# Kernel tuning notes

Measured on AMD Instinct MI355X. Metric: run time of the kernel, lower is better.

Reference implementation:

```python
import jax, jax.numpy as jnp
from jax import lax
import numpy as np

NEG = -1e9  # finite stand-in for -inf: keeps logaddexp grads NaN-free, exp underflows to 0
BLANK = 0
T_MAX, B, C = 256, 64, 8000
L_MAX = 32


def setup_inputs() -> dict:
    key = jax.random.key(0)
    k1, k2, k3, k4 = jax.random.split(key, 4)
    logits = jax.random.normal(k1, (T_MAX, B, C), dtype=jnp.float32)
    log_probs = jax.nn.log_softmax(logits, axis=-1)  # [T,B,C]
    targets = jax.random.randint(k2, (B, L_MAX), 1, C, dtype=jnp.int32)  # labels in [1,C), blank excluded
    input_lengths = jax.random.randint(k3, (B,), T_MAX // 2 + 1, T_MAX + 1, dtype=jnp.int32)
    target_lengths = jax.random.randint(k4, (B,), L_MAX // 2 + 1, L_MAX + 1, dtype=jnp.int32)
    return {"log_probs": log_probs, "targets": targets,
            "input_lengths": input_lengths, "target_lengths": target_lengths}


def _ctc_losses(log_probs, targets, input_lengths, target_lengths):
    T, Bb, Cc = log_probs.shape
    Lm = targets.shape[1]
    S = 2 * Lm + 1

    # extended targets: blank-interleaved labels, blank beyond 2L (matches torch buffer)
    lmask = jnp.arange(Lm)[None, :] < target_lengths[:, None]
    tgt = jnp.where(lmask, targets, BLANK)
    ext = jnp.full((Bb, S), BLANK, dtype=targets.dtype).at[:, 1::2].set(tgt)  # [B,S]

    ext_shift2 = jnp.concatenate(
        [jnp.full((Bb, 2), -1, dtype=ext.dtype), ext[:, :-2]], axis=1)
    skip = (ext != BLANK) & (ext != ext_shift2)  # [B,S]

    # emissions[t,b,s] = log_probs[t, b, ext[b,s]]
    emissions = jnp.take_along_axis(
        log_probs, jnp.broadcast_to(ext[None], (T, Bb, S)), axis=2)  # [T,B,S]

    # alpha init at t=0
    lp0 = log_probs[0]
    a0 = jnp.full((Bb, S), NEG, dtype=log_probs.dtype)
    a0 = a0.at[:, 0].set(lp0[:, BLANK])
    first_char = jnp.take_along_axis(lp0, ext[:, 1:2], axis=1)[:, 0]
    a0 = a0.at[:, 1].set(jnp.where(target_lengths > 0, first_char,
                                   jnp.full((Bb,), NEG, dtype=log_probs.dtype)))

    neg1 = jnp.full((Bb, 1), NEG, dtype=log_probs.dtype)
    neg2 = jnp.full((Bb, 2), NEG, dtype=log_probs.dtype)

    def step(alpha, em_t):
        p = jnp.logaddexp(alpha, jnp.concatenate([neg1, alpha[:, :-1]], axis=1))
        p = jnp.where(skip, jnp.logaddexp(p, jnp.concatenate([neg2, alpha[:, :-2]], axis=1)), p)
        new = p + em_t
        return new, new

    _, hist = lax.scan(step, a0, emissions[1:])
    alpha_hist = jnp.concatenate([a0[None], hist], axis=0)  # [T,B,S]

    final_alpha = alpha_hist[input_lengths - 1, jnp.arange(Bb)]  # [B,S]
    i_blank = 2 * target_lengths
    i_char = jnp.maximum(2 * target_lengths - 1, 0)
    v_blank = jnp.take_along_axis(final_alpha, i_blank[:, None], axis=1)[:, 0]
    v_char = jnp.take_along_axis(final_alpha, i_char[:, None], axis=1)[:, 0]
    total_log_prob = jnp.where(target_lengths > 0,
                               jnp.logaddexp(v_blank, v_char), v_blank)
    return -total_log_prob  # [B]


def reference(log_probs, targets, input_lengths, target_lengths):
    losses = _ctc_losses(log_probs, targets, input_lengths, target_lengths)
    safe_len = jnp.maximum(target_lengths, 1).astype(losses.dtype)
    return jnp.mean(losses / safe_len)  # reduction='mean'
```

## Files before the change

kernel.cpp:

```cpp
#include <hip/hip_runtime.h>
#include <cstdint>
#include <cstddef>


#define TMAX  256
#define BATCH 64
#define CNUM  8000
#define LMAX  32
#define SDIM  65
#define LOG2E 1.44269504088896340736f
#define LN2   0.69314718055994530942f
#define NEG2  (-1.0e9f * LOG2E)

__device__ __forceinline__ float hexp2(float x) { return __builtin_amdgcn_exp2f(x); }
__device__ __forceinline__ float hlog2(float x) { return __builtin_amdgcn_logf(x); }

__device__ __forceinline__ float lae3_log2(float a, float b, float c) {
    float m = fmaxf(fmaxf(a, b), c);
    float r = hexp2(a - m) + hexp2(b - m) + hexp2(c - m);
    return m + hlog2(r);
}

__global__ __launch_bounds__(256) void ctc_dp(
    const float* __restrict__ lp, const int* __restrict__ targets,
    const int* __restrict__ in_len, const int* __restrict__ tg_len,
    float* __restrict__ partial)
{
    const int b   = blockIdx.x;
    const int tid = threadIdx.x;
    const int Lb  = tg_len[b];
    const int Tb  = in_len[b];

    __shared__ float s_em[TMAX][LMAX + 1];

    {
        const int t = tid;
        const float* rowbase = lp + (size_t)t * (size_t)(BATCH * CNUM)
                                  + (size_t)b * CNUM;
        s_em[t][LMAX] = rowbase[0];
        #pragma unroll
        for (int k = 0; k < LMAX; ++k) {
            int lab = (k < Lb) ? targets[b * LMAX + k] : 0;
            s_em[t][k] = rowbase[lab];
        }
    }
    __syncthreads();
    if (tid >= 64) return;

    const int lane = tid;

    int  label = 0;
    bool skip  = false;
    if (lane & 1) {
        int k = lane >> 1;
        label = (k < Lb) ? targets[b * LMAX + k] : 0;
        int prev = (k >= 1) ? ((k - 1 < Lb) ? targets[b * LMAX + (k - 1)] : 0) : -1;
        skip = (label != 0) && (label != prev);
    }
    const bool use2 = skip && (lane >= 2);

    const int col = (lane & 1) ? (lane >> 1) : LMAX;

    float em0 = s_em[0][col];
    float a   = NEG2;
    if (lane == 0)            a = em0 * LOG2E;
    if (lane == 1 && Lb > 0)  a = em0 * LOG2E;
    float a64 = NEG2;

    const int steps = Tb - 1;
    float emc = s_em[1][col];
    for (int t = 1; t <= steps; ++t) {
        int tn = (t < TMAX - 1) ? (t + 1) : (TMAX - 1);
        float emn = s_em[tn][col];

        float em2  = emc * LOG2E;
        float em2b = __uint_as_float(
            __builtin_amdgcn_readfirstlane(__float_as_uint(em2)));

        float am1 = __shfl_up(a, 1, 64);
        float am2 = __shfl_up(a, 2, 64);
        am1 = (lane >= 1) ? am1 : NEG2;
        float am2p = use2 ? am2 : NEG2;

        float m64  = fmaxf(a64, a);
        float r64  = hexp2(a64 - m64) + hexp2(a - m64);
        float a64n = m64 + hlog2(r64) + em2b;

        a   = lae3_log2(a, am1, am2p) + em2;
        a64 = a64n;
        emc = emn;
    }

    int iB = 2 * Lb;
    int iC = iB - 1; if (iC < 0) iC = 0;
    float vB = (iB < 64) ? __shfl(a, iB, 64) : __shfl(a64, 63, 64);
    float vC = __shfl(a, iC, 64);

    if (lane == 0) {
        float tot2;
        if (Lb > 0) {
            float m = fmaxf(vB, vC);
            tot2 = m + hlog2(hexp2(vB - m) + hexp2(vC - m));
        } else {
            tot2 = vB;
        }
        float loss = -(tot2 * LN2);
        float sl   = (Lb > 0) ? (float)Lb : 1.0f;
        partial[b] = loss / sl;
    }
}

__global__ __launch_bounds__(64) void ctc_reduce(
    const float* __restrict__ partial, float* __restrict__ out)
{
    float v = partial[threadIdx.x];
    #pragma unroll
    for (int off = 32; off > 0; off >>= 1) v += __shfl_xor(v, off, 64);
    if (threadIdx.x == 0) out[0] = v * (1.0f / BATCH);
}

extern "C" void kernel_launch(void* const* d_in, const int* in_sizes, int n_in,
                              void* d_out, int out_size, void* d_ws, size_t ws_size,
                              hipStream_t stream) {
    const float* lp = (const float*)d_in[0];
    const int*   tg = (const int*)d_in[1];
    const int*   il = (const int*)d_in[2];
    const int*   tl = (const int*)d_in[3];
    float* partial  = (float*)d_ws;

    ctc_dp<<<dim3(BATCH), dim3(256), 0, stream>>>(lp, tg, il, tl, partial);
    ctc_reduce<<<dim3(1), dim3(64), 0, stream>>>(partial, (float*)d_out);
}
```

Before: 608.3 us.

## Pack blank and label states per lane and shift via DPP

Changes the state layout so each of the 64 lanes holds one blank state and one label state, instead of one extended-state slot per lane plus a separate tail value. The recurrence then needs only a single one-lane shift per time step, done with a DPP wave shift in place of two shfl_up permutes. Emissions are also multiplied by log2(e) once while being staged into shared memory, which takes that multiply out of the serial loop. The aim is a shorter critical path in the latency-bound time loop, at the cost of relying on the DPP wave_shr control being supported on this target.

```diff
diff --git a/kernel.cpp b/kernel.cpp
--- a/kernel.cpp
+++ b/kernel.cpp
@@ -7,7 +7,6 @@
 #define BATCH 64
 #define CNUM  8000
 #define LMAX  32
-#define SDIM  65
 #define LOG2E 1.44269504088896340736f
 #define LN2   0.69314718055994530942f
 #define NEG2  (-1.0e9f * LOG2E)
@@ -15,10 +14,10 @@
 __device__ __forceinline__ float hexp2(float x) { return __builtin_amdgcn_exp2f(x); }
 __device__ __forceinline__ float hlog2(float x) { return __builtin_amdgcn_logf(x); }
 
-__device__ __forceinline__ float lae3_log2(float a, float b, float c) {
-    float m = fmaxf(fmaxf(a, b), c);
-    float r = hexp2(a - m) + hexp2(b - m) + hexp2(c - m);
-    return m + hlog2(r);
+__device__ __forceinline__ float dpp_shr1(float x, float fill) {
+    int v = __builtin_amdgcn_update_dpp(
+        __float_as_int(fill), __float_as_int(x), 0x138, 0xf, 0xf, false);
+    return __int_as_float(v);
 }
 
 __global__ __launch_bounds__(256) void ctc_dp(
@@ -37,11 +36,11 @@
         const int t = tid;
         const float* rowbase = lp + (size_t)t * (size_t)(BATCH * CNUM)
                                   + (size_t)b * CNUM;
-        s_em[t][LMAX] = rowbase[0];
+        s_em[t][LMAX] = rowbase[0] * LOG2E;
         #pragma unroll
         for (int k = 0; k < LMAX; ++k) {
             int lab = (k < Lb) ? targets[b * LMAX + k] : 0;
-            s_em[t][k] = rowbase[lab];
+            s_em[t][k] = rowbase[lab] * LOG2E;
         }
     }
     __syncthreads();
@@ -49,52 +48,45 @@
 
     const int lane = tid;
 
-    int  label = 0;
-    bool skip  = false;
-    if (lane & 1) {
-        int k = lane >> 1;
-        label = (k < Lb) ? targets[b * LMAX + k] : 0;
-        int prev = (k >= 1) ? ((k - 1 < Lb) ? targets[b * LMAX + (k - 1)] : 0) : -1;
-        skip = (label != 0) && (label != prev);
+    int lab_k = (lane < Lb) ? targets[b * LMAX + lane] : 0;
+    int lab_p = (lane >= 1)
+                    ? ((lane - 1 < Lb) ? targets[b * LMAX + (lane - 1)] : 0)
+                    : -1;
+    const bool skip = (lab_k != 0) && (lab_k != lab_p);
+
+    const int colo = (lane < LMAX) ? lane : LMAX;
+
+    float ae = NEG2, ao = NEG2;
+    if (lane == 0) {
+        ae = s_em[0][LMAX];
+        if (Lb > 0) ao = s_em[0][0];
     }
-    const bool use2 = skip && (lane >= 2);
-
-    const int col = (lane & 1) ? (lane >> 1) : LMAX;
-
-    float em0 = s_em[0][col];
-    float a   = NEG2;
-    if (lane == 0)            a = em0 * LOG2E;
-    if (lane == 1 && Lb > 0)  a = em0 * LOG2E;
-    float a64 = NEG2;
 
     const int steps = Tb - 1;
-    float emc = s_em[1][col];
+    float eo_c = s_em[1][colo];
+    float eb_c = s_em[1][LMAX];
     for (int t = 1; t <= steps; ++t) {
         int tn = (t < TMAX - 1) ? (t + 1) : (TMAX - 1);
-        float emn = s_em[tn][col];
+        float eo_n = s_em[tn][colo];
+        float eb_n = s_em[tn][LMAX];
 
-        float em2  = emc * LOG2E;
-        float em2b = __uint_as_float(
-            __builtin_amdgcn_readfirstlane(__float_as_uint(em2)));
+        float po  = dpp_shr1(ao, NEG2);
+        float pos = skip ? po : NEG2;
 
-        float am1 = __shfl_up(a, 1, 64);
-        float am2 = __shfl_up(a, 2, 64);
-        am1 = (lane >= 1) ? am1 : NEG2;
-        float am2p = use2 ? am2 : NEG2;
+        float me = fmaxf(ae, po);
+        float re = hexp2(ae - me) + hexp2(po - me);
+        float ne = me + hlog2(re) + eb_c;
 
-        float m64  = fmaxf(a64, a);
-        float r64  = hexp2(a64 - m64) + hexp2(a - m64);
-        float a64n = m64 + hlog2(r64) + em2b;
+        float mo = fmaxf(fmaxf(ao, ae), pos);
+        float ro = hexp2(ao - mo) + hexp2(ae - mo) + hexp2(pos - mo);
+        float no = mo + hlog2(ro) + eo_c;
 
-        a   = lae3_log2(a, am1, am2p) + em2;
-        a64 = a64n;
-        emc = emn;
+        ae = ne; ao = no;
+        eo_c = eo_n; eb_c = eb_n;
     }
 
-    int iB = 2 * Lb;
-    int iC = iB - 1; if (iC < 0) iC = 0;
-    float vB = (iB < 64) ? __shfl(a, iB, 64) : __shfl(a64, 63, 64);
-    float vC = __shfl(a, iC, 64);
+    float vB = __shfl(ae, Lb, 64);
+    float vC = __shfl(ao, (Lb > 0) ? (Lb - 1) : 0, 64);
 
     if (lane == 0) {
         float tot2;
```

New measurement: 602.8 us. Within noise of the previous version (-0.9%).
